# Kernel optimization log

Measured on AMD Instinct MI355X. Metric: run time of the kernel, lower is better.

The kernel has to match this reference:

```python
import jax, jax.numpy as jnp
import numpy as np

T, B, I, H, L = 128, 64, 1024, 1024, 8


def setup_inputs() -> dict:
    key = jax.random.key(0)
    k0, k1, k2, k3, k4 = jax.random.split(key, 5)
    w_scale = 1.0 / np.sqrt(H)
    return {
        "inputs": jax.random.normal(k0, (T, B, I), dtype=jnp.float32),
        "Wih": jax.random.normal(k1, (L, 4, I, H), dtype=jnp.float32) * w_scale,
        "Whh": jax.random.normal(k2, (L, 4, H, H), dtype=jnp.float32) * w_scale,
        "bih": jax.random.normal(k3, (L, 4, H), dtype=jnp.float32),
        "bhh": jax.random.normal(k4, (L, 4, H), dtype=jnp.float32),
    }


def reference(inputs, Wih, Whh, bih, bhh):
    L_ = Wih.shape[0]
    B_ = inputs.shape[1]
    H_ = Wih.shape[-1]
    bias = bih + bhh  # [L,4,H]
    c0 = jnp.zeros((L_, B_, H_), dtype=inputs.dtype)
    h0 = jnp.zeros((L_, B_, H_), dtype=inputs.dtype)

    def step(carry, x_t):
        c, h = carry  # each [L,B,H]
        cur = x_t  # [B,I]
        cs, hs = [], []
        for j in range(L_):
            # gates: [4,B,H]
            gates = (jnp.einsum('bi,gih->gbh', cur, Wih[j])
                     + jnp.einsum('bk,gkh->gbh', h[j], Whh[j])
                     + bias[j][:, None, :])
            ig = jax.nn.sigmoid(gates[0])
            fg = jax.nn.sigmoid(gates[1])
            cg = jnp.tanh(gates[2])
            og = jax.nn.sigmoid(gates[3])
            cj = fg * c[j] + ig * cg
            hj = og * jnp.tanh(cj)
            cs.append(cj)
            hs.append(hj)
            cur = hj
        return (jnp.stack(cs), jnp.stack(hs)), None

    (c_fin, h_fin), _ = jax.lax.scan(step, (c0, h0), inputs)
    return h_fin[-1]  # [B,H] hidden state of last layer
```

## Files before the change

### kernel.cpp

```cpp
#include <hip/hip_runtime.h>


typedef __attribute__((ext_vector_type(8))) short short8;
typedef __attribute__((ext_vector_type(4))) float f32x4;

#define T_ 128
#define B_ 64
#define H_ 1024
#define L_ 8
#define SLAB 65536

__device__ __forceinline__ unsigned short f2bf(float f) {
    unsigned u = __builtin_bit_cast(unsigned, f);
    u += 0x7fff + ((u >> 16) & 1);
    return (unsigned short)(u >> 16);
}

__global__ void pack_weights(const float* __restrict__ Wih, const float* __restrict__ Whh,
                             unsigned short* __restrict__ packedW) {
    int tid = blockIdx.x * 256 + threadIdx.x;
    int lane = tid & 63;
    int kchunk = (tid >> 6) & 63;
    int ntile = (tid >> 12) & 255;
    int l = tid >> 20;
    int n = ntile * 16 + (lane & 15);
    int g = n >> 10;
    int h = n & 1023;
    int kbase = kchunk * 32 + ((lane >> 4) << 3);
    short8 v;
#pragma unroll
    for (int j = 0; j < 8; ++j) {
        int k = kbase + j;
        float w = (k < 1024) ? Wih[(((l * 4 + g) * 1024 + k) << 10) + h]
                             : Whh[(((l * 4 + g) * 1024 + (k - 1024)) << 10) + h];
        v[j] = (short)f2bf(w);
    }
    *(short8*)(packedW + (size_t)tid * 8) = v;
}

__global__ void prep_misc(const float* __restrict__ x, const float* __restrict__ bih,
                          const float* __restrict__ bhh, unsigned short* __restrict__ xA,
                          float* __restrict__ bias, float* __restrict__ c_state,
                          unsigned short* __restrict__ hA) {
    int tid = blockIdx.x * 256 + threadIdx.x;
    int ioct = tid & 127;
    int b = (tid >> 7) & 63;
    int t = tid >> 13;
    int i0 = ioct * 8;
    const float* src = x + ((size_t)(t * 64 + b) << 10) + i0;
    short8 v;
#pragma unroll
    for (int j = 0; j < 8; ++j) v[j] = (short)f2bf(src[j]);
    int kc = i0 >> 5;
    int q = (i0 >> 3) & 3;
    int mt = b >> 4;
    int m = b & 15;
    *(short8*)(xA + (size_t)t * SLAB + (((kc * 4 + mt) * 64 + q * 16 + m) << 3)) = v;

    if (tid < L_ * 4096) bias[tid] = bih[tid] + bhh[tid];
    if (tid < L_ * B_ * H_ / 2) { c_state[2 * tid] = 0.f; c_state[2 * tid + 1] = 0.f; }
    if (tid < 131072) *(short8*)(hA + (size_t)tid * 8) = (short8)0;
}

__global__ __launch_bounds__(256, 2)
void lstm_diag(const unsigned short* __restrict__ packedW,
               const unsigned short* __restrict__ xA,
               const float* __restrict__ bias,
               float* __restrict__ c_state,
               unsigned short* __restrict__ hA,
               float* __restrict__ out,
               int d, int lmin) {
    __shared__ float P[4 * 4 * 16 * 68];
    const int l = lmin + blockIdx.y;
    const int t = d - l;
    const int strip = blockIdx.x;
    const int tid = threadIdx.x;
    const int lane = tid & 63;
    const int kq = tid >> 6;
    const int m = lane & 15;
    const int q = lane >> 4;

    const unsigned short* slab0 = (l == 0) ? (xA + (size_t)t * SLAB)
                                           : (hA + (size_t)((t & 1) * L_ + (l - 1)) * SLAB);
    const unsigned short* slab1 = hA + (size_t)(((t + 1) & 1) * L_ + l) * SLAB;
    const unsigned short* A = (kq < 2) ? slab0 : slab1;
    const int kc0 = (kq & 1) * 16;

    const unsigned short* Bp0 = packedW + (((size_t)l * 256 + 0 * 64 + strip) * 32768)
                              + (size_t)(kq * 16) * 512 + lane * 8;
    const unsigned short* Bp1 = Bp0 + (size_t)64 * 32768;
    const unsigned short* Bp2 = Bp0 + (size_t)128 * 32768;
    const unsigned short* Bp3 = Bp0 + (size_t)192 * 32768;

    f32x4 acc[4][4];
#pragma unroll
    for (int g = 0; g < 4; ++g)
#pragma unroll
        for (int mt = 0; mt < 4; ++mt) acc[g][mt] = (f32x4)0.f;

#pragma unroll 2
    for (int kc = 0; kc < 16; ++kc) {
        short8 a[4];
#pragma unroll
        for (int mt = 0; mt < 4; ++mt)
            a[mt] = *(const short8*)(A + (((kc0 + kc) * 4 + mt) * 64 + lane) * 8);
        short8 b0 = *(const short8*)(Bp0 + kc * 512);
        short8 b1 = *(const short8*)(Bp1 + kc * 512);
        short8 b2 = *(const short8*)(Bp2 + kc * 512);
        short8 b3 = *(const short8*)(Bp3 + kc * 512);
#pragma unroll
        for (int mt = 0; mt < 4; ++mt) {
            acc[0][mt] = __builtin_amdgcn_mfma_f32_16x16x32_bf16(a[mt], b0, acc[0][mt], 0, 0, 0);
            acc[1][mt] = __builtin_amdgcn_mfma_f32_16x16x32_bf16(a[mt], b1, acc[1][mt], 0, 0, 0);
            acc[2][mt] = __builtin_amdgcn_mfma_f32_16x16x32_bf16(a[mt], b2, acc[2][mt], 0, 0, 0);
            acc[3][mt] = __builtin_amdgcn_mfma_f32_16x16x32_bf16(a[mt], b3, acc[3][mt], 0, 0, 0);
        }
    }

#pragma unroll
    for (int g = 0; g < 4; ++g)
#pragma unroll
        for (int mt = 0; mt < 4; ++mt)
            *(f32x4*)&P[((kq * 4 + g) * 16 + m) * 68 + mt * 16 + q * 4] = acc[g][mt];
    __syncthreads();

    {
        const int u = tid & 15;
        const int b0i = (tid >> 4) << 2;
        const int ug = strip * 16 + u;
        f32x4 G[4];
#pragma unroll
        for (int g = 0; g < 4; ++g) G[g] = (f32x4)0.f;
#pragma unroll
        for (int w = 0; w < 4; ++w)
#pragma unroll
            for (int g = 0; g < 4; ++g)
                G[g] += *(const f32x4*)&P[((w * 4 + g) * 16 + u) * 68 + b0i];
        const float* bs = bias + l * 4096;
        const float bi = bs[ug], bff = bs[1024 + ug], bc = bs[2048 + ug], bo = bs[3072 + ug];
        unsigned short* hslab = hA + (size_t)((t & 1) * L_ + l) * SLAB;
        const int hbase = ((ug >> 5) * 4) * 64 * 8 + (((ug >> 3) & 3) * 16) * 8 + (ug & 7);
#pragma unroll
        for (int rb = 0; rb < 4; ++rb) {
            int b = b0i + rb;
            float gi = G[0][rb] + bi;
            float gf = G[1][rb] + bff;
            float gc = G[2][rb] + bc;
            float go = G[3][rb] + bo;
            float ig = 1.f / (1.f + __expf(-gi));
            float fg = 1.f / (1.f + __expf(-gf));
            float cg = tanhf(gc);
            float og = 1.f / (1.f + __expf(-go));
            int cidx = ((l * 64 + b) << 10) + ug;
            float cnew = fg * c_state[cidx] + ig * cg;
            c_state[cidx] = cnew;
            float hnew = og * tanhf(cnew);
            hslab[hbase + ((b >> 4) * 64 + (b & 15)) * 8] = f2bf(hnew);
            if (l == 7 && t == 127) out[(b << 10) + ug] = hnew;
        }
    }
}

extern "C" void kernel_launch(void* const* d_in, const int* in_sizes, int n_in,
                              void* d_out, int out_size, void* d_ws, size_t ws_size,
                              hipStream_t stream) {
    const float* x   = (const float*)d_in[0];
    const float* Wih = (const float*)d_in[1];
    const float* Whh = (const float*)d_in[2];
    const float* bih = (const float*)d_in[3];
    const float* bhh = (const float*)d_in[4];
    float* out = (float*)d_out;

    char* ws = (char*)d_ws;
    unsigned short* packedW = (unsigned short*)ws;
    unsigned short* xA      = (unsigned short*)(ws + 134217728);
    float* bias             = (float*)(ws + 134217728 + 16777216);
    float* c_state          = (float*)(ws + 134217728 + 16777216 + 131072);
    unsigned short* hA      = (unsigned short*)(ws + 134217728 + 16777216 + 131072 + 2097152);

    hipLaunchKernelGGL(pack_weights, dim3(32768), dim3(256), 0, stream, Wih, Whh, packedW);
    hipLaunchKernelGGL(prep_misc, dim3(4096), dim3(256), 0, stream,
                       x, bih, bhh, xA, bias, c_state, hA);
    for (int d = 0; d <= 134; ++d) {
        int lmin = d > 127 ? d - 127 : 0;
        int lmax = d < 7 ? d : 7;
        hipLaunchKernelGGL(lstm_diag, dim3(64, lmax - lmin + 1), dim3(256), 0, stream,
                           packedW, xA, bias, c_state, hA, out, d, lmin);
    }
}
```

Before: 4.015 ms.

## Process eight timesteps per launch using in-kernel per-layer atomic barriers

Each launch now covers a block of eight timesteps per layer instead of one, cutting the wavefront launches from 135 to 23. Blocks of the same layer synchronise between timesteps through a spinning atomic counter. The h history buffer grows to 16 slots so the time-blocked diagonal stays correct, and the cell state is kept in registers across the eight steps. The spin barrier relies on all blocks of a layer being co-resident, it can deadlock or hit the spin timeout if they are not, and it adds a global atomic round trip per step.

```diff
diff --git a/kernel.cpp b/kernel.cpp
--- a/kernel.cpp
+++ b/kernel.cpp
@@ -8,6 +8,7 @@
 #define B_ 64
 #define H_ 1024
 #define L_ 8
+#define TB 8
 #define SLAB 65536
 
 __device__ __forceinline__ unsigned short f2bf(float f) {
@@ -41,7 +42,7 @@
 __global__ void prep_misc(const float* __restrict__ x, const float* __restrict__ bih,
                           const float* __restrict__ bhh, unsigned short* __restrict__ xA,
                           float* __restrict__ bias, float* __restrict__ c_state,
-                          unsigned short* __restrict__ hA) {
+                          unsigned short* __restrict__ hA, unsigned* __restrict__ bar) {
     int tid = blockIdx.x * 256 + threadIdx.x;
     int ioct = tid & 127;
     int b = (tid >> 7) & 63;
@@ -59,7 +60,8 @@
 
     if (tid < L_ * 4096) bias[tid] = bih[tid] + bhh[tid];
     if (tid < L_ * B_ * H_ / 2) { c_state[2 * tid] = 0.f; c_state[2 * tid + 1] = 0.f; }
-    if (tid < 131072) *(short8*)(hA + (size_t)tid * 8) = (short8)0;
+    *(short8*)(hA + (size_t)tid * 8) = (short8)0;
+    if (tid < 8) bar[tid * 64] = 0u;
 }
 
 __global__ __launch_bounds__(256, 2)
@@ -68,11 +70,12 @@
                const float* __restrict__ bias,
                float* __restrict__ c_state,
                unsigned short* __restrict__ hA,
+               unsigned* __restrict__ bar,
                float* __restrict__ out,
-               int d, int lmin) {
+               int D, int lmin) {
     __shared__ float P[4 * 4 * 16 * 68];
     const int l = lmin + blockIdx.y;
-    const int t = d - l;
+    const int tb = D - l;
     const int strip = blockIdx.x;
     const int tid = threadIdx.x;
     const int lane = tid & 63;
@@ -80,85 +83,111 @@
     const int m = lane & 15;
     const int q = lane >> 4;
 
-    const unsigned short* slab0 = (l == 0) ? (xA + (size_t)t * SLAB)
-                                           : (hA + (size_t)((t & 1) * L_ + (l - 1)) * SLAB);
-    const unsigned short* slab1 = hA + (size_t)(((t + 1) & 1) * L_ + l) * SLAB;
-    const unsigned short* A = (kq < 2) ? slab0 : slab1;
     const int kc0 = (kq & 1) * 16;
-
     const unsigned short* Bp0 = packedW + (((size_t)l * 256 + 0 * 64 + strip) * 32768)
                               + (size_t)(kq * 16) * 512 + lane * 8;
     const unsigned short* Bp1 = Bp0 + (size_t)64 * 32768;
     const unsigned short* Bp2 = Bp0 + (size_t)128 * 32768;
     const unsigned short* Bp3 = Bp0 + (size_t)192 * 32768;
 
-    f32x4 acc[4][4];
-#pragma unroll
-    for (int g = 0; g < 4; ++g)
-#pragma unroll
-        for (int mt = 0; mt < 4; ++mt) acc[g][mt] = (f32x4)0.f;
+    const int u = tid & 15;
+    const int b0i = (tid >> 4) << 2;
+    const int ug = strip * 16 + u;
+    const float* bs = bias + l * 4096;
+    const float bi = bs[ug], bff = bs[1024 + ug], bc = bs[2048 + ug], bo = bs[3072 + ug];
+    float creg[4];
+#pragma unroll
+    for (int rb = 0; rb < 4; ++rb)
+        creg[rb] = c_state[((l * 64 + b0i + rb) << 10) + ug];
+    const int hbase = ((ug >> 5) * 4) * 64 * 8 + (((ug >> 3) & 3) * 16) * 8 + (ug & 7);
+    unsigned* barl = bar + l * 64;
+
+    for (int i = 0; i < TB; ++i) {
+        const int t = tb * TB + i;
+        const unsigned short* slab0 = (l == 0)
+            ? (xA + (size_t)t * SLAB)
+            : (hA + (size_t)((t & 15) * L_ + (l - 1)) * SLAB);
+        const unsigned short* slab1 = hA + (size_t)((((t + 15) & 15)) * L_ + l) * SLAB;
+        const unsigned short* A = (kq < 2) ? slab0 : slab1;
+
+        f32x4 acc[4][4];
+#pragma unroll
+        for (int g = 0; g < 4; ++g)
+#pragma unroll
+            for (int mt = 0; mt < 4; ++mt) acc[g][mt] = (f32x4)0.f;
 
 #pragma unroll 2
-    for (int kc = 0; kc < 16; ++kc) {
-        short8 a[4];
-#pragma unroll
-        for (int mt = 0; mt < 4; ++mt)
-            a[mt] = *(const short8*)(A + (((kc0 + kc) * 4 + mt) * 64 + lane) * 8);
-        short8 b0 = *(const short8*)(Bp0 + kc * 512);
-        short8 b1 = *(const short8*)(Bp1 + kc * 512);
-        short8 b2 = *(const short8*)(Bp2 + kc * 512);
-        short8 b3 = *(const short8*)(Bp3 + kc * 512);
-#pragma unroll
-        for (int mt = 0; mt < 4; ++mt) {
-            acc[0][mt] = __builtin_amdgcn_mfma_f32_16x16x32_bf16(a[mt], b0, acc[0][mt], 0, 0, 0);
-            acc[1][mt] = __builtin_amdgcn_mfma_f32_16x16x32_bf16(a[mt], b1, acc[1][mt], 0, 0, 0);
-            acc[2][mt] = __builtin_amdgcn_mfma_f32_16x16x32_bf16(a[mt], b2, acc[2][mt], 0, 0, 0);
-            acc[3][mt] = __builtin_amdgcn_mfma_f32_16x16x32_bf16(a[mt], b3, acc[3][mt], 0, 0, 0);
+        for (int kc = 0; kc < 16; ++kc) {
+            short8 a[4];
+#pragma unroll
+            for (int mt = 0; mt < 4; ++mt)
+                a[mt] = *(const short8*)(A + (((kc0 + kc) * 4 + mt) * 64 + lane) * 8);
+            short8 b0 = *(const short8*)(Bp0 + kc * 512);
+            short8 b1 = *(const short8*)(Bp1 + kc * 512);
+            short8 b2 = *(const short8*)(Bp2 + kc * 512);
+            short8 b3 = *(const short8*)(Bp3 + kc * 512);
+#pragma unroll
+            for (int mt = 0; mt < 4; ++mt) {
+                acc[0][mt] = __builtin_amdgcn_mfma_f32_16x16x32_bf16(a[mt], b0, acc[0][mt], 0, 0, 0);
+                acc[1][mt] = __builtin_amdgcn_mfma_f32_16x16x32_bf16(a[mt], b1, acc[1][mt], 0, 0, 0);
+                acc[2][mt] = __builtin_amdgcn_mfma_f32_16x16x32_bf16(a[mt], b2, acc[2][mt], 0, 0, 0);
+                acc[3][mt] = __builtin_amdgcn_mfma_f32_16x16x32_bf16(a[mt], b3, acc[3][mt], 0, 0, 0);
+            }
+        }
+
+#pragma unroll
+        for (int g = 0; g < 4; ++g)
+#pragma unroll
+            for (int mt = 0; mt < 4; ++mt)
+                *(f32x4*)&P[((kq * 4 + g) * 16 + m) * 68 + mt * 16 + q * 4] = acc[g][mt];
+        __syncthreads();
+
+        {
+            f32x4 G[4];
+#pragma unroll
+            for (int g = 0; g < 4; ++g) G[g] = (f32x4)0.f;
+#pragma unroll
+            for (int w = 0; w < 4; ++w)
+#pragma unroll
+                for (int g = 0; g < 4; ++g)
+                    G[g] += *(const f32x4*)&P[((w * 4 + g) * 16 + u) * 68 + b0i];
+            unsigned short* hslab = hA + (size_t)((t & 15) * L_ + l) * SLAB;
+#pragma unroll
+            for (int rb = 0; rb < 4; ++rb) {
+                int b = b0i + rb;
+                float gi = G[0][rb] + bi;
+                float gf = G[1][rb] + bff;
+                float gc = G[2][rb] + bc;
+                float go = G[3][rb] + bo;
+                float ig = 1.f / (1.f + __expf(-gi));
+                float fg = 1.f / (1.f + __expf(-gf));
+                float cg = tanhf(gc);
+                float og = 1.f / (1.f + __expf(-go));
+                float cnew = fg * creg[rb] + ig * cg;
+                creg[rb] = cnew;
+                float hnew = og * tanhf(cnew);
+                hslab[hbase + ((b >> 4) * 64 + (b & 15)) * 8] = f2bf(hnew);
+                if (l == 7 && t == 127) out[(b << 10) + ug] = hnew;
+            }
+        }
+
+        if (i < TB - 1) {
+            __syncthreads();
+            if (tid == 0) {
+                __hip_atomic_fetch_add(barl, 1u, __ATOMIC_RELEASE, __HIP_MEMORY_SCOPE_AGENT);
+                unsigned tgt = 64u * (7 * tb + i + 1);
+                unsigned spin = 0;
+                while (__hip_atomic_load(barl, __ATOMIC_RELAXED, __HIP_MEMORY_SCOPE_AGENT) < tgt
+                       && ++spin < (1u << 24))
+                    __builtin_amdgcn_s_sleep(2);
+            }
+            __syncthreads();
         }
     }
 
 #pragma unroll
-    for (int g = 0; g < 4; ++g)
-#pragma unroll
-        for (int mt = 0; mt < 4; ++mt)
-            *(f32x4*)&P[((kq * 4 + g) * 16 + m) * 68 + mt * 16 + q * 4] = acc[g][mt];
-    __syncthreads();
-
-    {
-        const int u = tid & 15;
-        const int b0i = (tid >> 4) << 2;
-        const int ug = strip * 16 + u;
-        f32x4 G[4];
-#pragma unroll
-        for (int g = 0; g < 4; ++g) G[g] = (f32x4)0.f;
-#pragma unroll
-        for (int w = 0; w < 4; ++w)
-#pragma unroll
-            for (int g = 0; g < 4; ++g)
-                G[g] += *(const f32x4*)&P[((w * 4 + g) * 16 + u) * 68 + b0i];
-        const float* bs = bias + l * 4096;
-        const float bi = bs[ug], bff = bs[1024 + ug], bc = bs[2048 + ug], bo = bs[3072 + ug];
-        unsigned short* hslab = hA + (size_t)((t & 1) * L_ + l) * SLAB;
-        const int hbase = ((ug >> 5) * 4) * 64 * 8 + (((ug >> 3) & 3) * 16) * 8 + (ug & 7);
-#pragma unroll
-        for (int rb = 0; rb < 4; ++rb) {
-            int b = b0i + rb;
-            float gi = G[0][rb] + bi;
-            float gf = G[1][rb] + bff;
-            float gc = G[2][rb] + bc;
-            float go = G[3][rb] + bo;
-            float ig = 1.f / (1.f + __expf(-gi));
-            float fg = 1.f / (1.f + __expf(-gf));
-            float cg = tanhf(gc);
-            float og = 1.f / (1.f + __expf(-go));
-            int cidx = ((l * 64 + b) << 10) + ug;
-            float cnew = fg * c_state[cidx] + ig * cg;
-            c_state[cidx] = cnew;
-            float hnew = og * tanhf(cnew);
-            hslab[hbase + ((b >> 4) * 64 + (b & 15)) * 8] = f2bf(hnew);
-            if (l == 7 && t == 127) out[(b << 10) + ug] = hnew;
-        }
-    }
+    for (int rb = 0; rb < 4; ++rb)
+        c_state[((l * 64 + b0i + rb) << 10) + ug] = creg[rb];
 }
 
 extern "C" void kernel_launch(void* const* d_in, const int* in_sizes, int n_in,
@@ -174,17 +203,18 @@
     char* ws = (char*)d_ws;
     unsigned short* packedW = (unsigned short*)ws;
     unsigned short* xA      = (unsigned short*)(ws + 134217728);
-    float* bias             = (float*)(ws + 134217728 + 16777216);
-    float* c_state          = (float*)(ws + 134217728 + 16777216 + 131072);
-    unsigned short* hA      = (unsigned short*)(ws + 134217728 + 16777216 + 131072 + 2097152);
+    float* bias             = (float*)(ws + 150994944);
+    float* c_state          = (float*)(ws + 151126016);
+    unsigned short* hA      = (unsigned short*)(ws + 153223168);
+    unsigned* bar           = (unsigned*)(ws + 170000384);
 
     hipLaunchKernelGGL(pack_weights, dim3(32768), dim3(256), 0, stream, Wih, Whh, packedW);
     hipLaunchKernelGGL(prep_misc, dim3(4096), dim3(256), 0, stream,
-                       x, bih, bhh, xA, bias, c_state, hA);
-    for (int d = 0; d <= 134; ++d) {
-        int lmin = d > 127 ? d - 127 : 0;
-        int lmax = d < 7 ? d : 7;
+                       x, bih, bhh, xA, bias, c_state, hA, bar);
+    for (int D = 0; D <= 22; ++D) {
+        int lmin = D > 15 ? D - 15 : 0;
+        int lmax = D < 7 ? D : 7;
         hipLaunchKernelGGL(lstm_diag, dim3(64, lmax - lmin + 1), dim3(256), 0, stream,
-                           packedW, xA, bias, c_state, hA, out, d, lmin);
+                           packedW, xA, bias, c_state, hA, bar, out, D, lmin);
     }
 }
```

New measurement: 5.803 ms. +44.5%, slower.
